# Optimization experiments

Measured on AMD Instinct MI355X. Metric: run time of the kernel, lower is better.

## Reference

```python
import jax, jax.numpy as jnp
import numpy as np

BS, N, D_IN, HID, D_OUT = 16, 256, 128, 128, 128


def setup_inputs() -> dict:
    key = jax.random.key(0)
    ks = jax.random.split(key, 10)
    s = 0.02
    return {
        "x": jax.random.normal(ks[0], (BS, N, D_IN), dtype=jnp.float32),
        "adj": jax.random.randint(ks[1], (BS, N, N), 0, 2, dtype=jnp.int32),
        "W_fc": jax.random.normal(ks[2], (D_IN, HID), dtype=jnp.float32) * s,
        "b_fc": jnp.zeros((HID,), dtype=jnp.float32),
        "W_a1": jax.random.normal(ks[3], (2 * HID, HID), dtype=jnp.float32) * s,
        "b_a1": jnp.zeros((HID,), dtype=jnp.float32),
        "w_a2": jax.random.normal(ks[4], (HID,), dtype=jnp.float32) * s,
        "b_a2": jnp.zeros((), dtype=jnp.float32),
        "W_out": jax.random.normal(ks[5], (HID, D_OUT), dtype=jnp.float32) * s,
        "b_out": jnp.zeros((D_OUT,), dtype=jnp.float32),
    }


def reference(x, adj, W_fc, b_fc, W_a1, b_a1, w_a2, b_a2, W_out, b_out):
    # h = fc(x): (bs, n, hid)
    h = jnp.einsum("bnd,dh->bnh", x, W_fc) + b_fc
    # attn first layer on concat([h_i, h_j]) decomposes into two half-projections
    # (same math as Linear(2*hid, hid) on the concatenated pair features).
    a_i = jnp.einsum("bnh,hk->bnk", h, W_a1[:HID])  # contribution of h_i
    a_j = jnp.einsum("bnh,hk->bnk", h, W_a1[HID:])  # contribution of h_j
    pre = a_i[:, :, None, :] + a_j[:, None, :, :] + b_a1  # (bs, n, n, hid)
    e = jnp.einsum("bijk,k->bij", jax.nn.relu(pre), w_a2) + b_a2  # (bs, n, n)
    e = jnp.where(adj == 0, jnp.float32(-1e9), e)
    attn = jax.nn.softmax(e, axis=-1)
    h_prime = jnp.einsum("bij,bjh->bih", attn, h)
    out = jnp.einsum("bih,ho->bio", h_prime, W_out) + b_out
    return out
```

## Files before the change

kernel.cpp:

```cpp
#include <hip/hip_runtime.h>

#define BS  16
#define NN  256
#define HID 128

__device__ __forceinline__ int xcd_swz(int bid) {
    return (bid & 7) * 64 + (bid >> 3);
}

__global__ __launch_bounds__(512, 4) void gat_k1(
    const float* __restrict__ x, const float* __restrict__ W_fc,
    const float* __restrict__ b_fc, const float* __restrict__ W_a1,
    const float* __restrict__ b_a1, const float* __restrict__ W_out,
    float* __restrict__ aiT, float* __restrict__ ajT, float* __restrict__ g)
{
    __shared__ __align__(16) float xs[8][HID];
    __shared__ __align__(16) float hs[8][HID];
    __shared__ __align__(16) float red[4][3][8][HID];

    const int tid = threadIdx.x;
    const int k   = tid & 127;
    const int q   = tid >> 7;
    const int swz = xcd_swz(blockIdx.x);
    const int r0  = swz * 8;
    const int b   = r0 >> 8;
    const int n0  = r0 & 255;

    for (int t = tid; t < 8 * HID; t += 512)
        xs[t >> 7][t & 127] = x[r0 * HID + t];
    __syncthreads();

    {
        float acc[8] = {0,0,0,0,0,0,0,0};
        const int dq = 32 * q;
        #pragma unroll 2
        for (int d = 0; d < 32; d += 4) {
            float w[4];
            #pragma unroll
            for (int t = 0; t < 4; ++t) w[t] = W_fc[(dq + d + t) * HID + k];
            #pragma unroll
            for (int r = 0; r < 8; ++r) {
                const float4 xv = *(const float4*)&xs[r][dq + d];
                acc[r] += xv.x * w[0] + xv.y * w[1] + xv.z * w[2] + xv.w * w[3];
            }
        }
        #pragma unroll
        for (int r = 0; r < 8; ++r) red[q][0][r][k] = acc[r];
    }
    __syncthreads();

    {
        const float bf = b_fc[k];
        #pragma unroll
        for (int r2 = 0; r2 < 2; ++r2) {
            const int r = 2 * q + r2;
            hs[r][k] = (red[0][0][r][k] + red[1][0][r][k])
                     + (red[2][0][r][k] + red[3][0][r][k]) + bf;
        }
    }
    __syncthreads();

    {
        float ai_a[8] = {0,0,0,0,0,0,0,0};
        float aj_a[8] = {0,0,0,0,0,0,0,0};
        float g_a[8]  = {0,0,0,0,0,0,0,0};
        const int dq = 32 * q;
        #pragma unroll 2
        for (int d = 0; d < 32; d += 4) {
            float wi[4], wj[4], wo[4];
            #pragma unroll
            for (int t = 0; t < 4; ++t) {
                wi[t] = W_a1[(dq + d + t) * HID + k];
                wj[t] = W_a1[(HID + dq + d + t) * HID + k];
                wo[t] = W_out[(dq + d + t) * HID + k];
            }
            #pragma unroll
            for (int r = 0; r < 8; ++r) {
                const float4 hv = *(const float4*)&hs[r][dq + d];
                ai_a[r] += hv.x * wi[0] + hv.y * wi[1] + hv.z * wi[2] + hv.w * wi[3];
                aj_a[r] += hv.x * wj[0] + hv.y * wj[1] + hv.z * wj[2] + hv.w * wj[3];
                g_a[r]  += hv.x * wo[0] + hv.y * wo[1] + hv.z * wo[2] + hv.w * wo[3];
            }
        }
        #pragma unroll
        for (int r = 0; r < 8; ++r) {
            red[q][0][r][k] = ai_a[r];
            red[q][1][r][k] = aj_a[r];
            red[q][2][r][k] = g_a[r];
        }
    }
    __syncthreads();

    {
        const int is_aj = q >> 1;
        const int rb4   = (q & 1) * 4;
        const float bias = is_aj ? 0.f : b_a1[k];
        float4 v;
        v.x = (red[0][is_aj][rb4 + 0][k] + red[1][is_aj][rb4 + 0][k])
            + (red[2][is_aj][rb4 + 0][k] + red[3][is_aj][rb4 + 0][k]) + bias;
        v.y = (red[0][is_aj][rb4 + 1][k] + red[1][is_aj][rb4 + 1][k])
            + (red[2][is_aj][rb4 + 1][k] + red[3][is_aj][rb4 + 1][k]) + bias;
        v.z = (red[0][is_aj][rb4 + 2][k] + red[1][is_aj][rb4 + 2][k])
            + (red[2][is_aj][rb4 + 2][k] + red[3][is_aj][rb4 + 2][k]) + bias;
        v.w = (red[0][is_aj][rb4 + 3][k] + red[1][is_aj][rb4 + 3][k])
            + (red[2][is_aj][rb4 + 3][k] + red[3][is_aj][rb4 + 3][k]) + bias;
        float* dst = (is_aj ? ajT : aiT) + (b * HID + k) * NN + n0 + rb4;
        *(float4*)dst = v;

        #pragma unroll
        for (int r2 = 0; r2 < 2; ++r2) {
            const int r = 2 * q + r2;
            g[(r0 + r) * HID + k] = (red[0][2][r][k] + red[1][2][r][k])
                                  + (red[2][2][r][k] + red[3][2][r][k]);
        }
    }
}

__global__ __launch_bounds__(512, 4) void gat_k2(
    const float* __restrict__ aiT, const float* __restrict__ ajT,
    const float* __restrict__ g,  const int* __restrict__ adj,
    const float* __restrict__ w_a2, const float* __restrict__ b_a2,
    const float* __restrict__ b_out, float* __restrict__ out)
{
    __shared__ __align__(16) float4 aiwp[HID][4];
    __shared__ __align__(16) float  buf[2][8][NN];
    __shared__ __align__(16) float  ep[8][NN];

    const int tid = threadIdx.x;
    const int swz = xcd_swz(blockIdx.x);
    const int b   = swz >> 5;
    const int i0  = (swz & 31) * 8;
    const int wv  = tid >> 6, lane = tid & 63;

    {
        const int kk = tid >> 2, rp2 = tid & 3;
        const float* ar = aiT + (b * HID + kk) * NN + i0 + 2 * rp2;
        float4 v;
        v.x = ar[0];
        v.y = ar[1];
        v.z = w_a2[kk];
        v.w = 0.f;
        aiwp[kk][rp2] = v;
    }

    const int4 am = *(const int4*)(adj + (b * NN + i0 + wv) * NN + 4 * lane);
    __syncthreads();

    const int kh = wv >> 2, rp = wv & 3;
    {
        const float* ajp = ajT + (b * HID + kh * 64) * NN + 4 * lane;
        float4 acc0 = {0,0,0,0}, acc1 = {0,0,0,0}, saw = {0,0,0,0};
        const int kb = kh * 64;
        #pragma unroll 8
        for (int t = 0; t < 64; ++t) {
            const float4 a4 = *(const float4*)(ajp + t * NN);
            const float4 aw = aiwp[kb + t][rp];
            saw.x  = __builtin_fmaf(a4.x, aw.z, saw.x);
            saw.y  = __builtin_fmaf(a4.y, aw.z, saw.y);
            saw.z  = __builtin_fmaf(a4.z, aw.z, saw.z);
            saw.w  = __builtin_fmaf(a4.w, aw.z, saw.w);
            acc0.x = __builtin_fmaf(fmaxf(aw.x, -a4.x), aw.z, acc0.x);
            acc0.y = __builtin_fmaf(fmaxf(aw.x, -a4.y), aw.z, acc0.y);
            acc0.z = __builtin_fmaf(fmaxf(aw.x, -a4.z), aw.z, acc0.z);
            acc0.w = __builtin_fmaf(fmaxf(aw.x, -a4.w), aw.z, acc0.w);
            acc1.x = __builtin_fmaf(fmaxf(aw.y, -a4.x), aw.z, acc1.x);
            acc1.y = __builtin_fmaf(fmaxf(aw.y, -a4.y), aw.z, acc1.y);
            acc1.z = __builtin_fmaf(fmaxf(aw.y, -a4.z), aw.z, acc1.z);
            acc1.w = __builtin_fmaf(fmaxf(aw.y, -a4.w), aw.z, acc1.w);
        }
        const float4 e0 = {acc0.x + saw.x, acc0.y + saw.y,
                           acc0.z + saw.z, acc0.w + saw.w};
        const float4 e1 = {acc1.x + saw.x, acc1.y + saw.y,
                           acc1.z + saw.z, acc1.w + saw.w};
        *(float4*)&buf[kh][2 * rp + 0][4 * lane] = e0;
        *(float4*)&buf[kh][2 * rp + 1][4 * lane] = e1;
    }
    __syncthreads();

    {
        const float ba2 = b_a2[0];
        const float4 u = *(const float4*)&buf[0][wv][4 * lane];
        const float4 v = *(const float4*)&buf[1][wv][4 * lane];
        const float e0 = am.x ? u.x + v.x + ba2 : -1e9f;
        const float e1 = am.y ? u.y + v.y + ba2 : -1e9f;
        const float e2 = am.z ? u.z + v.z + ba2 : -1e9f;
        const float e3 = am.w ? u.w + v.w + ba2 : -1e9f;
        float m = fmaxf(fmaxf(e0, e1), fmaxf(e2, e3));
        #pragma unroll
        for (int off = 32; off; off >>= 1) m = fmaxf(m, __shfl_xor(m, off));
        const float p0 = __expf(e0 - m), p1 = __expf(e1 - m);
        const float p2 = __expf(e2 - m), p3 = __expf(e3 - m);
        float s = (p0 + p1) + (p2 + p3);
        #pragma unroll
        for (int off = 32; off; off >>= 1) s += __shfl_xor(s, off);
        const float inv = 1.f / s;
        const float4 pv = {p0 * inv, p1 * inv, p2 * inv, p3 * inv};
        *(float4*)&ep[wv][4 * lane] = pv;
    }
    __syncthreads();

    float* red = &buf[0][0][0];
    const int qh = wv & 3, rh = wv >> 2;
    {
        float2 o[4];
        #pragma unroll
        for (int r = 0; r < 4; ++r) { o[r].x = 0.f; o[r].y = 0.f; }
        const int jb = qh * 64;
        const float* gb = g + (b * NN + jb) * HID + 2 * lane;
        #pragma unroll 2
        for (int jq = 0; jq < 64; jq += 4) {
            const float2 g0 = *(const float2*)(gb + (jq + 0) * HID);
            const float2 g1 = *(const float2*)(gb + (jq + 1) * HID);
            const float2 g2 = *(const float2*)(gb + (jq + 2) * HID);
            const float2 g3 = *(const float2*)(gb + (jq + 3) * HID);
            #pragma unroll
            for (int r = 0; r < 4; ++r) {
                const float4 pv = *(const float4*)&ep[rh * 4 + r][jb + jq];
                o[r].x += pv.x * g0.x + pv.y * g1.x + pv.z * g2.x + pv.w * g3.x;
                o[r].y += pv.x * g0.y + pv.y * g1.y + pv.z * g2.y + pv.w * g3.y;
            }
        }
        #pragma unroll
        for (int r = 0; r < 4; ++r)
            *(float2*)&red[(qh * 8 + rh * 4 + r) * HID + 2 * lane] = o[r];
    }
    __syncthreads();

    {
        const int k = tid & 127, qh2 = tid >> 7;
        const float bo = b_out[k];
        #pragma unroll
        for (int r2 = 0; r2 < 2; ++r2) {
            const int r = 2 * qh2 + r2;
            out[(b * NN + i0 + r) * HID + k] =
                (red[(0 + r) * HID + k]  + red[(8 + r) * HID + k]) +
                (red[(16 + r) * HID + k] + red[(24 + r) * HID + k]) + bo;
        }
    }
}

extern "C" void kernel_launch(void* const* d_in, const int* in_sizes, int n_in,
                              void* d_out, int out_size, void* d_ws, size_t ws_size,
                              hipStream_t stream) {
    const float* x     = (const float*)d_in[0];
    const int*   adj   = (const int*)  d_in[1];
    const float* W_fc  = (const float*)d_in[2];
    const float* b_fc  = (const float*)d_in[3];
    const float* W_a1  = (const float*)d_in[4];
    const float* b_a1  = (const float*)d_in[5];
    const float* w_a2  = (const float*)d_in[6];
    const float* b_a2  = (const float*)d_in[7];
    const float* W_out = (const float*)d_in[8];
    const float* b_out = (const float*)d_in[9];
    float* out = (float*)d_out;

    float* ws  = (float*)d_ws;
    float* aiT = ws;
    float* ajT = ws + BS * NN * HID;
    float* g   = ws + 2 * BS * NN * HID;

    gat_k1<<<BS * NN / 8, 512, 0, stream>>>(x, W_fc, b_fc, W_a1, b_a1, W_out,
                                            aiT, ajT, g);
    gat_k2<<<BS * (NN / 8), 512, 0, stream>>>(aiT, ajT, g, adj, w_a2, b_a2,
                                              b_out, out);
}
```

Baseline: 41.35 us.

## Move W_out projection from per-node precompute to after attention aggregation in k2

The first kernel now writes h directly instead of projecting it to g = h·W_out. The second kernel aggregates attention over h and then applies W_out to the 8 aggregated rows per block, reusing the aiwp shared buffer for staging. This cuts a third of the projection work and the shared reduction footprint in k1. In exchange, k2 gains an extra barrier and a serial 128-step matvec per thread that reads W_out from global memory.

```diff
diff --git a/kernel.cpp b/kernel.cpp
--- a/kernel.cpp
+++ b/kernel.cpp
@@ -11,12 +11,12 @@
 __global__ __launch_bounds__(512, 4) void gat_k1(
     const float* __restrict__ x, const float* __restrict__ W_fc,
     const float* __restrict__ b_fc, const float* __restrict__ W_a1,
-    const float* __restrict__ b_a1, const float* __restrict__ W_out,
-    float* __restrict__ aiT, float* __restrict__ ajT, float* __restrict__ g)
+    const float* __restrict__ b_a1,
+    float* __restrict__ aiT, float* __restrict__ ajT, float* __restrict__ h)
 {
     __shared__ __align__(16) float xs[8][HID];
     __shared__ __align__(16) float hs[8][HID];
-    __shared__ __align__(16) float red[4][3][8][HID];
+    __shared__ __align__(16) float red[4][2][8][HID];
 
     const int tid = threadIdx.x;
     const int k   = tid & 127;
@@ -54,8 +54,10 @@
         #pragma unroll
         for (int r2 = 0; r2 < 2; ++r2) {
             const int r = 2 * q + r2;
-            hs[r][k] = (red[0][0][r][k] + red[1][0][r][k])
-                     + (red[2][0][r][k] + red[3][0][r][k]) + bf;
+            const float hv = (red[0][0][r][k] + red[1][0][r][k])
+                           + (red[2][0][r][k] + red[3][0][r][k]) + bf;
+            hs[r][k] = hv;
+            h[(r0 + r) * HID + k] = hv;
         }
     }
     __syncthreads();
@@ -63,30 +65,26 @@
     {
         float ai_a[8] = {0,0,0,0,0,0,0,0};
         float aj_a[8] = {0,0,0,0,0,0,0,0};
-        float g_a[8]  = {0,0,0,0,0,0,0,0};
         const int dq = 32 * q;
         #pragma unroll 2
         for (int d = 0; d < 32; d += 4) {
-            float wi[4], wj[4], wo[4];
+            float wi[4], wj[4];
             #pragma unroll
             for (int t = 0; t < 4; ++t) {
                 wi[t] = W_a1[(dq + d + t) * HID + k];
                 wj[t] = W_a1[(HID + dq + d + t) * HID + k];
-                wo[t] = W_out[(dq + d + t) * HID + k];
             }
             #pragma unroll
             for (int r = 0; r < 8; ++r) {
                 const float4 hv = *(const float4*)&hs[r][dq + d];
                 ai_a[r] += hv.x * wi[0] + hv.y * wi[1] + hv.z * wi[2] + hv.w * wi[3];
                 aj_a[r] += hv.x * wj[0] + hv.y * wj[1] + hv.z * wj[2] + hv.w * wj[3];
-                g_a[r]  += hv.x * wo[0] + hv.y * wo[1] + hv.z * wo[2] + hv.w * wo[3];
             }
         }
         #pragma unroll
         for (int r = 0; r < 8; ++r) {
             red[q][0][r][k] = ai_a[r];
             red[q][1][r][k] = aj_a[r];
-            red[q][2][r][k] = g_a[r];
         }
     }
     __syncthreads();
@@ -106,21 +104,15 @@
             + (red[2][is_aj][rb4 + 3][k] + red[3][is_aj][rb4 + 3][k]) + bias;
         float* dst = (is_aj ? ajT : aiT) + (b * HID + k) * NN + n0 + rb4;
         *(float4*)dst = v;
-
-        #pragma unroll
-        for (int r2 = 0; r2 < 2; ++r2) {
-            const int r = 2 * q + r2;
-            g[(r0 + r) * HID + k] = (red[0][2][r][k] + red[1][2][r][k])
-                                  + (red[2][2][r][k] + red[3][2][r][k]);
-        }
     }
 }
 
 __global__ __launch_bounds__(512, 4) void gat_k2(
     const float* __restrict__ aiT, const float* __restrict__ ajT,
-    const float* __restrict__ g,  const int* __restrict__ adj,
+    const float* __restrict__ h,  const int* __restrict__ adj,
     const float* __restrict__ w_a2, const float* __restrict__ b_a2,
-    const float* __restrict__ b_out, float* __restrict__ out)
+    const float* __restrict__ W_out, const float* __restrict__ b_out,
+    float* __restrict__ out)
 {
     __shared__ __align__(16) float4 aiwp[HID][4];
     __shared__ __align__(16) float  buf[2][8][NN];
@@ -206,18 +198,18 @@
         #pragma unroll
         for (int r = 0; r < 4; ++r) { o[r].x = 0.f; o[r].y = 0.f; }
         const int jb = qh * 64;
-        const float* gb = g + (b * NN + jb) * HID + 2 * lane;
+        const float* hb = h + (b * NN + jb) * HID + 2 * lane;
         #pragma unroll 2
         for (int jq = 0; jq < 64; jq += 4) {
-            const float2 g0 = *(const float2*)(gb + (jq + 0) * HID);
-            const float2 g1 = *(const float2*)(gb + (jq + 1) * HID);
-            const float2 g2 = *(const float2*)(gb + (jq + 2) * HID);
-            const float2 g3 = *(const float2*)(gb + (jq + 3) * HID);
+            const float2 h0 = *(const float2*)(hb + (jq + 0) * HID);
+            const float2 h1 = *(const float2*)(hb + (jq + 1) * HID);
+            const float2 h2 = *(const float2*)(hb + (jq + 2) * HID);
+            const float2 h3 = *(const float2*)(hb + (jq + 3) * HID);
             #pragma unroll
             for (int r = 0; r < 4; ++r) {
                 const float4 pv = *(const float4*)&ep[rh * 4 + r][jb + jq];
-                o[r].x += pv.x * g0.x + pv.y * g1.x + pv.z * g2.x + pv.w * g3.x;
-                o[r].y += pv.x * g0.y + pv.y * g1.y + pv.z * g2.y + pv.w * g3.y;
+                o[r].x += pv.x * h0.x + pv.y * h1.x + pv.z * h2.x + pv.w * h3.x;
+                o[r].y += pv.x * h0.y + pv.y * h1.y + pv.z * h2.y + pv.w * h3.y;
             }
         }
         #pragma unroll
@@ -226,16 +218,35 @@
     }
     __syncthreads();
 
+    float* hp = (float*)&aiwp[0][0];
     {
         const int k = tid & 127, qh2 = tid >> 7;
-        const float bo = b_out[k];
         #pragma unroll
         for (int r2 = 0; r2 < 2; ++r2) {
             const int r = 2 * qh2 + r2;
-            out[(b * NN + i0 + r) * HID + k] =
+            hp[r * HID + k] =
                 (red[(0 + r) * HID + k]  + red[(8 + r) * HID + k]) +
-                (red[(16 + r) * HID + k] + red[(24 + r) * HID + k]) + bo;
-        }
+                (red[(16 + r) * HID + k] + red[(24 + r) * HID + k]);
+        }
+    }
+    __syncthreads();
+
+    {
+        const int k = tid & 127, q4 = tid >> 7;
+        const float bo = b_out[k];
+        float o0 = bo, o1 = bo;
+        #pragma unroll 2
+        for (int d0 = 0; d0 < HID; d0 += 4) {
+            float w[4];
+            #pragma unroll
+            for (int t = 0; t < 4; ++t) w[t] = W_out[(d0 + t) * HID + k];
+            const float4 hA = *(const float4*)&hp[(2 * q4 + 0) * HID + d0];
+            const float4 hB = *(const float4*)&hp[(2 * q4 + 1) * HID + d0];
+            o0 += hA.x * w[0] + hA.y * w[1] + hA.z * w[2] + hA.w * w[3];
+            o1 += hB.x * w[0] + hB.y * w[1] + hB.z * w[2] + hB.w * w[3];
+        }
+        out[(b * NN + i0 + 2 * q4 + 0) * HID + k] = o0;
+        out[(b * NN + i0 + 2 * q4 + 1) * HID + k] = o1;
     }
 }
 
@@ -257,10 +268,10 @@
     float* ws  = (float*)d_ws;
     float* aiT = ws;
     float* ajT = ws + BS * NN * HID;
-    float* g   = ws + 2 * BS * NN * HID;
-
-    gat_k1<<<BS * NN / 8, 512, 0, stream>>>(x, W_fc, b_fc, W_a1, b_a1, W_out,
-                                            aiT, ajT, g);
-    gat_k2<<<BS * (NN / 8), 512, 0, stream>>>(aiT, ajT, g, adj, w_a2, b_a2,
-                                              b_out, out);
-}
+    float* hbuf= ws + 2 * BS * NN * HID;
+
+    gat_k1<<<BS * NN / 8, 512, 0, stream>>>(x, W_fc, b_fc, W_a1, b_a1,
+                                            aiT, ajT, hbuf);
+    gat_k2<<<BS * (NN / 8), 512, 0, stream>>>(aiT, ajT, hbuf, adj, w_a2, b_a2,
+                                              W_out, b_out, out);
+}
```

After: 42.50 us. 2.8% more time.
